# Optimization experiments

Measured on AMD Instinct MI355X. Metric: run time of the kernel, lower is better.

## Reference

```python
import jax, jax.numpy as jnp
import numpy as np

B, S, E, L, H, FF, CB = 16, 1000, 512, 4, 8, 2048, 4096
DH = E // H

def _ln(x, g, b):
    m = x.mean(-1, keepdims=True)
    v = ((x - m) ** 2).mean(-1, keepdims=True)
    return (x - m) / jnp.sqrt(v + 1e-5) * g + b

def setup_inputs() -> dict:
    key = jax.random.key(0)
    cnt = [0]
    def rn(shape, s=0.02):
        cnt[0] += 1
        return jax.random.normal(jax.random.fold_in(key, cnt[0]), shape, jnp.float32) * s
    inp = {}
    inp['noisy_tokens'] = jax.random.randint(jax.random.fold_in(key, 999), (B, S), 0, CB, dtype=jnp.int32)
    inp['codebook'] = rn((CB, E), 1.0)
    # sinusoidal positional encoding, as in _create_positional_encoding
    pe = np.zeros((S, E), np.float32)
    pos = np.arange(S, dtype=np.float32)[:, None]
    div = np.exp(np.arange(0, E, 2, dtype=np.float32) * (-np.log(10000.0) / E))
    pe[:, 0::2] = np.sin(pos * div)
    pe[:, 1::2] = np.cos(pos * div)
    inp['pos_enc'] = jnp.asarray(pe)[None]  # [1,S,E]
    # transformer encoder layers (stacked over L)
    inp['qkv_w'] = rn((L, 3 * E, E)); inp['qkv_b'] = jnp.zeros((L, 3 * E))
    inp['out_w'] = rn((L, E, E));     inp['out_b'] = jnp.zeros((L, E))
    inp['ln1_g'] = jnp.ones((L, E));  inp['ln1_b'] = jnp.zeros((L, E))
    inp['ln2_g'] = jnp.ones((L, E));  inp['ln2_b'] = jnp.zeros((L, E))
    inp['ff1_w'] = rn((L, FF, E));    inp['ff1_b'] = jnp.zeros((L, FF))
    inp['ff2_w'] = rn((L, E, FF));    inp['ff2_b'] = jnp.zeros((L, E))
    inp['fin_g'] = jnp.ones((E,));    inp['fin_b'] = jnp.zeros((E,))
    # post_process: Linear, LN, GELU, Linear
    inp['pp1_w'] = rn((E, E)); inp['pp1_b'] = jnp.zeros((E,))
    inp['pp_ln_g'] = jnp.ones((E,)); inp['pp_ln_b'] = jnp.zeros((E,))
    inp['pp2_w'] = rn((E, E)); inp['pp2_b'] = jnp.zeros((E,))
    inp['res_w'] = jnp.float32(0.1)
    # feature_to_codebook: Linear, LN, GELU, Linear (codebook_dim == E)
    inp['fc1_w'] = rn((E, E)); inp['fc1_b'] = jnp.zeros((E,))
    inp['fc_ln_g'] = jnp.ones((E,)); inp['fc_ln_b'] = jnp.zeros((E,))
    inp['fc2_w'] = rn((E, E)); inp['fc2_b'] = jnp.zeros((E,))
    return inp

def reference(noisy_tokens, codebook, pos_enc, qkv_w, qkv_b, out_w, out_b,
              ln1_g, ln1_b, ln2_g, ln2_b, ff1_w, ff1_b, ff2_w, ff2_b,
              fin_g, fin_b, pp1_w, pp1_b, pp_ln_g, pp_ln_b, pp2_w, pp2_b,
              res_w, fc1_w, fc1_b, fc_ln_g, fc_ln_b, fc2_w, fc2_b):
    gelu = lambda z: jax.nn.gelu(z, approximate=False)
    # token embedding (codebook_projection is Identity) + positional encoding
    x = codebook[noisy_tokens] + pos_enc            # [B,S,E]
    # pre-norm transformer encoder (dropout=0 / eval)
    y = x
    for l in range(L):
        h = _ln(y, ln1_g[l], ln1_b[l])
        qkv = h @ qkv_w[l].T + qkv_b[l]             # [B,S,3E]
        q, k, v = jnp.split(qkv, 3, axis=-1)
        q = q.reshape(B, S, H, DH); k = k.reshape(B, S, H, DH); v = v.reshape(B, S, H, DH)
        scores = jnp.einsum('bqhd,bkhd->bhqk', q, k) / jnp.sqrt(jnp.float32(DH))
        attn = jax.nn.softmax(scores, axis=-1)
        ctx = jnp.einsum('bhqk,bkhd->bqhd', attn, v).reshape(B, S, E)
        y = y + (ctx @ out_w[l].T + out_b[l])
        h2 = _ln(y, ln2_g[l], ln2_b[l])
        y = y + (gelu(h2 @ ff1_w[l].T + ff1_b[l]) @ ff2_w[l].T + ff2_b[l])
    y = _ln(y, fin_g, fin_b)
    # post_process + residual
    pp = gelu(_ln(y @ pp1_w.T + pp1_b, pp_ln_g, pp_ln_b)) @ pp2_w.T + pp2_b
    enhanced = x + res_w * pp
    # feature_to_codebook
    fc = gelu(_ln(enhanced @ fc1_w.T + fc1_b, fc_ln_g, fc_ln_b)) @ fc2_w.T + fc2_b  # [B,S,E]
    # quantize: nearest neighbour in codebook (cdist + argmin)
    flat = fc.reshape(-1, E)
    d2 = (jnp.sum(flat ** 2, -1, keepdims=True)
          - 2.0 * flat @ codebook.T
          + jnp.sum(codebook ** 2, -1))            # [B*S, CB]
    tokens = jnp.argmin(d2, axis=-1).reshape(B, S)
    return fc, tokens
```

## Files before the change

### kernel.cpp

```cpp
#include <hip/hip_runtime.h>
#include <hip/hip_bf16.h>
#include <math.h>

#define NTOK 16000
#define E    512
#define FFD  2048
#define CBN  4096
#define SEQ  1000
#define NH   8
#define VLD  1008

typedef __hip_bfloat16 bf16;
typedef __attribute__((ext_vector_type(8))) short short8;
typedef __attribute__((ext_vector_type(4))) float f32x4;

__device__ __forceinline__ float gelu_f(float v) {
    return 0.5f * v * (1.0f + erff(v * 0.70710678118654752f));
}

__device__ __forceinline__ void split_store(float v, bf16* hi, bf16* lo, size_t idx) {
    bf16 h = __float2bfloat16(v);
    hi[idx] = h;
    lo[idx] = __float2bfloat16(v - __bfloat162float(h));
}

__device__ __forceinline__ void t2_ins(float v, int c, float& v1, int& c1, float& v2, int& c2) {
    const bool b1 = (v < v1) || (v == v1 && c < c1);
    const bool b2 = (v < v2) || (v == v2 && c < c2);
    if (b1) { v2 = v1; c2 = c1; v1 = v; c1 = c; }
    else if (b2) { v2 = v; c2 = c; }
}

__global__ __launch_bounds__(128) void embed_kernel(const int* __restrict__ tok,
                                                    const float* __restrict__ cb,
                                                    const float* __restrict__ pe,
                                                    float* __restrict__ y) {
    const int row = blockIdx.x;
    const int s = row % SEQ;
    const int t = tok[row];
    const int c = threadIdx.x * 4;
    const float4 cv = *(const float4*)(cb + (size_t)t * E + c);
    const float4 pv = *(const float4*)(pe + (size_t)s * E + c);
    *(float4*)(y + (size_t)row * E + c) =
        make_float4(cv.x + pv.x, cv.y + pv.y, cv.z + pv.z, cv.w + pv.w);
}

__global__ __launch_bounds__(256) void split_w(const float* __restrict__ src, int ld,
                                               int cols_log2, int n,
                                               bf16* __restrict__ hi, bf16* __restrict__ lo) {
    const int i = blockIdx.x * 256 + threadIdx.x;
    if (i >= n) return;
    const int r = i >> cols_log2;
    const int c = i & ((1 << cols_log2) - 1);
    const float v = src[(size_t)r * ld + c];
    split_store(v, hi, lo, i);
}

template<int GELU>
__global__ __launch_bounds__(256) void ln_planes(const float* __restrict__ in,
                                                 bf16* __restrict__ hi, bf16* __restrict__ lo,
                                                 const float* __restrict__ g,
                                                 const float* __restrict__ b) {
    const int lane = threadIdx.x & 63;
    const int row = blockIdx.x * 4 + (threadIdx.x >> 6);
    const float* p = in + (size_t)row * E;
    const float4 v0 = *(const float4*)(p + lane * 4);
    const float4 v1 = *(const float4*)(p + 256 + lane * 4);
    float sum = v0.x + v0.y + v0.z + v0.w + v1.x + v1.y + v1.z + v1.w;
    float sq = v0.x * v0.x + v0.y * v0.y + v0.z * v0.z + v0.w * v0.w
             + v1.x * v1.x + v1.y * v1.y + v1.z * v1.z + v1.w * v1.w;
#pragma unroll
    for (int m = 1; m < 64; m <<= 1) {
        sum += __shfl_xor(sum, m);
        sq += __shfl_xor(sq, m);
    }
    const float mean = sum * (1.0f / 512.0f);
    const float var = sq * (1.0f / 512.0f) - mean * mean;
    const float rstd = rsqrtf(var + 1e-5f);
    const float4 g0 = *(const float4*)(g + lane * 4);
    const float4 g1 = *(const float4*)(g + 256 + lane * 4);
    const float4 b0 = *(const float4*)(b + lane * 4);
    const float4 b1 = *(const float4*)(b + 256 + lane * 4);
    const size_t base = (size_t)row * E;
    float o;
    const float vv0[4] = {v0.x, v0.y, v0.z, v0.w};
    const float gg0[4] = {g0.x, g0.y, g0.z, g0.w};
    const float bb0[4] = {b0.x, b0.y, b0.z, b0.w};
    const float vv1[4] = {v1.x, v1.y, v1.z, v1.w};
    const float gg1[4] = {g1.x, g1.y, g1.z, g1.w};
    const float bb1[4] = {b1.x, b1.y, b1.z, b1.w};
#pragma unroll
    for (int t = 0; t < 4; ++t) {
        o = (vv0[t] - mean) * rstd * gg0[t] + bb0[t];
        if (GELU) o = gelu_f(o);
        split_store(o, hi, lo, base + lane * 4 + t);
        o = (vv1[t] - mean) * rstd * gg1[t] + bb1[t];
        if (GELU) o = gelu_f(o);
        split_store(o, hi, lo, base + 256 + lane * 4 + t);
    }
}

template<int OUT>
__global__ __launch_bounds__(256) void gemm_split(
    const bf16* __restrict__ Ah, const bf16* __restrict__ Al, int lda,
    const bf16* __restrict__ Wh, const bf16* __restrict__ Wl, int ldw,
    const float* __restrict__ bias,
    float* __restrict__ C, int ldc,
    bf16* __restrict__ Ohi, bf16* __restrict__ Olo, int ldp,
    const int* __restrict__ noisy, const float* __restrict__ cb,
    const float* __restrict__ pe, const float* __restrict__ resw,
    int K) {
    __shared__ short Ash[2][128][40];
    __shared__ short Wsh[2][128][40];
    const int tid = threadIdx.x;
    const int rowBase = blockIdx.y * 128;
    const int colBase = blockIdx.x * 128;
    const int wave = tid >> 6, lane = tid & 63;
    const int wm = (wave & 1) * 64, wn = (wave >> 1) * 64;
    const int lm = lane & 15;
    const int q8 = (lane >> 4) * 8;
    const int r0 = tid >> 2;
    const int kq = (tid & 3) * 8;

    f32x4 acc[4][4];
#pragma unroll
    for (int i = 0; i < 4; ++i)
#pragma unroll
        for (int j = 0; j < 4; ++j)
            acc[i][j] = (f32x4){0.f, 0.f, 0.f, 0.f};

    for (int k0 = 0; k0 < K; k0 += 32) {
        __syncthreads();
        {
            const size_t a0 = (size_t)(rowBase + r0) * lda + k0 + kq;
            const size_t a1 = (size_t)(rowBase + r0 + 64) * lda + k0 + kq;
            const size_t w0 = (size_t)(colBase + r0) * ldw + k0 + kq;
            const size_t w1 = (size_t)(colBase + r0 + 64) * ldw + k0 + kq;
            *(short8*)&Ash[0][r0][kq]      = *(const short8*)(Ah + a0);
            *(short8*)&Ash[0][r0 + 64][kq] = *(const short8*)(Ah + a1);
            *(short8*)&Ash[1][r0][kq]      = *(const short8*)(Al + a0);
            *(short8*)&Ash[1][r0 + 64][kq] = *(const short8*)(Al + a1);
            *(short8*)&Wsh[0][r0][kq]      = *(const short8*)(Wh + w0);
            *(short8*)&Wsh[0][r0 + 64][kq] = *(const short8*)(Wh + w1);
            *(short8*)&Wsh[1][r0][kq]      = *(const short8*)(Wl + w0);
            *(short8*)&Wsh[1][r0 + 64][kq] = *(const short8*)(Wl + w1);
        }
        __syncthreads();
        short8 ah[4], al[4], wh[4], wl[4];
#pragma unroll
        for (int i = 0; i < 4; ++i) {
            ah[i] = *(const short8*)&Ash[0][wm + i * 16 + lm][q8];
            al[i] = *(const short8*)&Ash[1][wm + i * 16 + lm][q8];
            wh[i] = *(const short8*)&Wsh[0][wn + i * 16 + lm][q8];
            wl[i] = *(const short8*)&Wsh[1][wn + i * 16 + lm][q8];
        }
#pragma unroll
        for (int i = 0; i < 4; ++i)
#pragma unroll
            for (int j = 0; j < 4; ++j)
                acc[i][j] = __builtin_amdgcn_mfma_f32_16x16x32_bf16(ah[i], wh[j], acc[i][j], 0, 0, 0);
#pragma unroll
        for (int i = 0; i < 4; ++i)
#pragma unroll
            for (int j = 0; j < 4; ++j)
                acc[i][j] = __builtin_amdgcn_mfma_f32_16x16x32_bf16(ah[i], wl[j], acc[i][j], 0, 0, 0);
#pragma unroll
        for (int i = 0; i < 4; ++i)
#pragma unroll
            for (int j = 0; j < 4; ++j)
                acc[i][j] = __builtin_amdgcn_mfma_f32_16x16x32_bf16(al[i], wh[j], acc[i][j], 0, 0, 0);
    }

    float bv[4];
#pragma unroll
    for (int j = 0; j < 4; ++j)
        bv[j] = bias ? bias[colBase + wn + j * 16 + lm] : 0.f;
    float scv = 0.f;
    if (OUT == 3) scv = resw[0];
#pragma unroll
    for (int i = 0; i < 4; ++i) {
#pragma unroll
        for (int reg = 0; reg < 4; ++reg) {
            const int r = rowBase + wm + i * 16 + (lane >> 4) * 4 + reg;
            int tok = 0, srow = 0;
            if (OUT == 3) { tok = noisy[r]; srow = r % SEQ; }
#pragma unroll
            for (int j = 0; j < 4; ++j) {
                const int col = colBase + wn + j * 16 + lm;
                float v = acc[i][j][reg] + bv[j];
                if (OUT == 0) {
                    C[(size_t)r * ldc + col] = v;
                } else if (OUT == 1) {
                    float* cp = C + (size_t)r * ldc + col;
                    *cp = *cp + v;
                } else if (OUT == 2) {
                    v = gelu_f(v);
                    split_store(v, Ohi, Olo, (size_t)r * ldp + col);
                } else if (OUT == 3) {
                    const float xv = cb[(size_t)tok * E + col] + pe[(size_t)srow * E + col];
                    v = xv + scv * v;
                    split_store(v, Ohi, Olo, (size_t)r * ldp + col);
                } else {
                    split_store(v, Ohi, Olo, (size_t)r * ldp + col);
                }
            }
        }
    }
}

__global__ __launch_bounds__(256) void vtrans(const bf16* __restrict__ vh_src,
                                              const bf16* __restrict__ vl_src,
                                              bf16* __restrict__ vth,
                                              bf16* __restrict__ vtl) {
    __shared__ short T[64][72];
    const int tid = threadIdx.x;
    const int st = blockIdx.x;
    const int bh = blockIdx.y;
    const int b = bh >> 3, h = bh & 7;
    const int sr = tid >> 2, dq = (tid & 3) * 16;
    const int s_g = st * 64 + sr;
    const int od = tid >> 3;
    const int osq = (tid & 7) * 8;
#pragma unroll
    for (int p = 0; p < 2; ++p) {
        const short* src = (const short*)(p ? vl_src : vh_src);
        short* dst = (short*)(p ? vtl : vth);
        short8 a0 = {0, 0, 0, 0, 0, 0, 0, 0};
        short8 a1 = {0, 0, 0, 0, 0, 0, 0, 0};
        if (s_g < SEQ) {
            const short* sp = src + (size_t)(b * SEQ + s_g) * 1536 + 1024 + h * 64 + dq;
            a0 = *(const short8*)sp;
            a1 = *(const short8*)(sp + 8);
        }
        __syncthreads();
#pragma unroll
        for (int j = 0; j < 8; ++j) T[dq + j][sr] = a0[j];
#pragma unroll
        for (int j = 0; j < 8; ++j) T[dq + 8 + j][sr] = a1[j];
        __syncthreads();
        const int scol = st * 64 + osq;
        if (scol + 8 <= VLD) {
            const short8 o0 = *(const short8*)&T[od][osq];
            const short8 o1 = *(const short8*)&T[od + 32][osq];
            *(short8*)(dst + (size_t)(bh * 64 + od) * VLD + scol) = o0;
            *(short8*)(dst + (size_t)(bh * 64 + od + 32) * VLD + scol) = o1;
        }
    }
}

__global__ __launch_bounds__(256) void attn_mfma(const bf16* __restrict__ qkh,
                                                 const bf16* __restrict__ qkl,
                                                 const bf16* __restrict__ vth,
                                                 const bf16* __restrict__ vtl,
                                                 bf16* __restrict__ chi,
                                                 bf16* __restrict__ clo) {
    __shared__ short QPs[2][64][72];
    __shared__ short Ks[2][64][72];
    __shared__ short Vs[2][64][72];
    const int tid = threadIdx.x;
    const int qt = blockIdx.x, bh = blockIdx.y;
    const int b = bh >> 3, h = bh & 7;
    const int wave = tid >> 6, lane = tid & 63;
    const int lm = lane & 15, g = lane >> 4, q8 = g * 8;
    const int wq = wave * 16;
    const int r0 = tid >> 2, kq = (tid & 3) * 16;

    {
        const int q = qt * 64 + r0;
        short8 z = {0, 0, 0, 0, 0, 0, 0, 0};
        short8 a0 = z, a1 = z, b0 = z, b1 = z;
        if (q < SEQ) {
            const size_t base = (size_t)(b * SEQ + q) * 1536 + h * 64 + kq;
            a0 = *(const short8*)((const short*)qkh + base);
            a1 = *(const short8*)((const short*)qkh + base + 8);
            b0 = *(const short8*)((const short*)qkl + base);
            b1 = *(const short8*)((const short*)qkl + base + 8);
        }
        *(short8*)&QPs[0][r0][kq] = a0; *(short8*)&QPs[0][r0][kq + 8] = a1;
        *(short8*)&QPs[1][r0][kq] = b0; *(short8*)&QPs[1][r0][kq + 8] = b1;
    }
    __syncthreads();
    short8 qfh[2], qfl[2];
#pragma unroll
    for (int t = 0; t < 2; ++t) {
        qfh[t] = *(const short8*)&QPs[0][wq + lm][t * 32 + q8];
        qfl[t] = *(const short8*)&QPs[1][wq + lm][t * 32 + q8];
    }

    float m_i[4] = {-3e38f, -3e38f, -3e38f, -3e38f};
    float l_i[4] = {0.f, 0.f, 0.f, 0.f};
    f32x4 o[4];
#pragma unroll
    for (int dt = 0; dt < 4; ++dt) o[dt] = (f32x4){0.f, 0.f, 0.f, 0.f};

    for (int kb = 0; kb < SEQ; kb += 64) {
        __syncthreads();
        {
            const int kr = kb + r0;
            short8 z = {0, 0, 0, 0, 0, 0, 0, 0};
            short8 a0 = z, a1 = z, b0 = z, b1 = z;
            if (kr < SEQ) {
                const size_t base = (size_t)(b * SEQ + kr) * 1536 + 512 + h * 64 + kq;
                a0 = *(const short8*)((const short*)qkh + base);
                a1 = *(const short8*)((const short*)qkh + base + 8);
                b0 = *(const short8*)((const short*)qkl + base);
                b1 = *(const short8*)((const short*)qkl + base + 8);
            }
            *(short8*)&Ks[0][r0][kq] = a0; *(short8*)&Ks[0][r0][kq + 8] = a1;
            *(short8*)&Ks[1][r0][kq] = b0; *(short8*)&Ks[1][r0][kq + 8] = b1;
            const size_t vbase = (size_t)(bh * 64 + r0) * VLD + kb + kq;
            short8 v0 = z, v1 = z, w0 = z, w1 = z;
            if (kb + kq + 8 <= VLD) {
                v0 = *(const short8*)((const short*)vth + vbase);
                w0 = *(const short8*)((const short*)vtl + vbase);
            }
            if (kb + kq + 16 <= VLD) {
                v1 = *(const short8*)((const short*)vth + vbase + 8);
                w1 = *(const short8*)((const short*)vtl + vbase + 8);
            }
            *(short8*)&Vs[0][r0][kq] = v0; *(short8*)&Vs[0][r0][kq + 8] = v1;
            *(short8*)&Vs[1][r0][kq] = w0; *(short8*)&Vs[1][r0][kq + 8] = w1;
        }
        __syncthreads();
        f32x4 sac[4];
#pragma unroll
        for (int j = 0; j < 4; ++j) sac[j] = (f32x4){0.f, 0.f, 0.f, 0.f};
#pragma unroll
        for (int t = 0; t < 2; ++t) {
#pragma unroll
            for (int j = 0; j < 4; ++j) {
                const short8 kh = *(const short8*)&Ks[0][j * 16 + lm][t * 32 + q8];
                const short8 kl = *(const short8*)&Ks[1][j * 16 + lm][t * 32 + q8];
                sac[j] = __builtin_amdgcn_mfma_f32_16x16x32_bf16(qfh[t], kh, sac[j], 0, 0, 0);
                sac[j] = __builtin_amdgcn_mfma_f32_16x16x32_bf16(qfh[t], kl, sac[j], 0, 0, 0);
                sac[j] = __builtin_amdgcn_mfma_f32_16x16x32_bf16(qfl[t], kh, sac[j], 0, 0, 0);
            }
        }
        float alpha_v[4];
#pragma unroll
        for (int reg = 0; reg < 4; ++reg) {
            float sv[4];
            float rm = -3e38f;
#pragma unroll
            for (int j = 0; j < 4; ++j) {
                const int kc = kb + j * 16 + lm;
                float s = sac[j][reg] * 0.125f;
                s = (kc < SEQ) ? s : -3e38f;
                sv[j] = s;
                rm = fmaxf(rm, s);
            }
#pragma unroll
            for (int m = 1; m < 16; m <<= 1) rm = fmaxf(rm, __shfl_xor(rm, m));
            const float mn = fmaxf(m_i[reg], rm);
            const float al = expf(m_i[reg] - mn);
            float rs = 0.f;
            const int prow = wq + g * 4 + reg;
#pragma unroll
            for (int j = 0; j < 4; ++j) {
                const float pv = expf(sv[j] - mn);
                rs += pv;
                bf16 phb = __float2bfloat16(pv);
                bf16 plb = __float2bfloat16(pv - __bfloat162float(phb));
                QPs[0][prow][j * 16 + lm] = *reinterpret_cast<short*>(&phb);
                QPs[1][prow][j * 16 + lm] = *reinterpret_cast<short*>(&plb);
            }
#pragma unroll
            for (int m = 1; m < 16; m <<= 1) rs += __shfl_xor(rs, m);
            l_i[reg] = l_i[reg] * al + rs;
            m_i[reg] = mn;
            alpha_v[reg] = al;
        }
        const f32x4 av = {alpha_v[0], alpha_v[1], alpha_v[2], alpha_v[3]};
#pragma unroll
        for (int dt = 0; dt < 4; ++dt) o[dt] *= av;
        __syncthreads();
#pragma unroll
        for (int t = 0; t < 2; ++t) {
            const short8 ph = *(const short8*)&QPs[0][wq + lm][t * 32 + q8];
            const short8 pl = *(const short8*)&QPs[1][wq + lm][t * 32 + q8];
#pragma unroll
            for (int dt = 0; dt < 4; ++dt) {
                const short8 vh = *(const short8*)&Vs[0][dt * 16 + lm][t * 32 + q8];
                const short8 vl = *(const short8*)&Vs[1][dt * 16 + lm][t * 32 + q8];
                o[dt] = __builtin_amdgcn_mfma_f32_16x16x32_bf16(ph, vh, o[dt], 0, 0, 0);
                o[dt] = __builtin_amdgcn_mfma_f32_16x16x32_bf16(ph, vl, o[dt], 0, 0, 0);
                o[dt] = __builtin_amdgcn_mfma_f32_16x16x32_bf16(pl, vh, o[dt], 0, 0, 0);
            }
        }
    }
#pragma unroll
    for (int reg = 0; reg < 4; ++reg) {
        const int q = qt * 64 + wq + g * 4 + reg;
        if (q < SEQ) {
            const float inv = 1.0f / l_i[reg];
#pragma unroll
            for (int dt = 0; dt < 4; ++dt) {
                const size_t idx = (size_t)(b * SEQ + q) * E + h * 64 + dt * 16 + lm;
                split_store(o[dt][reg] * inv, chi, clo, idx);
            }
        }
    }
}

__global__ __launch_bounds__(256) void cbnorm_kernel(const float* __restrict__ cb,
                                                     float* __restrict__ out) {
    const int lane = threadIdx.x & 63;
    const int row = blockIdx.x * 4 + (threadIdx.x >> 6);
    const float* p = cb + (size_t)row * E;
    const float4 v0 = *(const float4*)(p + lane * 4);
    const float4 v1 = *(const float4*)(p + 256 + lane * 4);
    float sq = v0.x * v0.x + v0.y * v0.y + v0.z * v0.z + v0.w * v0.w
             + v1.x * v1.x + v1.y * v1.y + v1.z * v1.z + v1.w * v1.w;
#pragma unroll
    for (int m = 1; m < 64; m <<= 1) sq += __shfl_xor(sq, m);
    if (lane == 0) out[row] = sq;
}

__global__ __launch_bounds__(256) void argmin_mfma(
    const bf16* __restrict__ Ah, const bf16* __restrict__ Al,
    const bf16* __restrict__ Wh, const bf16* __restrict__ Wl,
    const float* __restrict__ cbn, float4* __restrict__ part) {
    __shared__ __align__(16) short sbuf[2][2][128][40];
    float4* mrg = reinterpret_cast<float4*>(&sbuf[0][0][0][0]);
    const int tid = threadIdx.x;
    const int rowBase = blockIdx.y * 128;
    const int wave = tid >> 6, lane = tid & 63;
    const int wm = wave * 32;
    const int lm = lane & 15;
    const int g = lane >> 4;
    const int q8 = g * 8;
    const int r0 = tid >> 2;
    const int kq = (tid & 3) * 8;
    const int own_row = tid >> 1;
    const int own_half = tid & 1;

    float rv1 = 3e38f, rv2 = 3e38f;
    int rc1 = 0x7fffffff, rc2 = 0x7fffffff;

    for (int ct = 0; ct < 4; ++ct) {
        const int colBase = blockIdx.x * 512 + ct * 128;
        f32x4 acc[2][8];
#pragma unroll
        for (int i = 0; i < 2; ++i)
#pragma unroll
            for (int j = 0; j < 8; ++j)
                acc[i][j] = (f32x4){0.f, 0.f, 0.f, 0.f};

        for (int k0 = 0; k0 < E; k0 += 32) {
            __syncthreads();
            {
                const size_t a0 = (size_t)(rowBase + r0) * E + k0 + kq;
                const size_t a1 = (size_t)(rowBase + r0 + 64) * E + k0 + kq;
                const size_t w0 = (size_t)(colBase + r0) * E + k0 + kq;
                const size_t w1 = (size_t)(colBase + r0 + 64) * E + k0 + kq;
                *(short8*)&sbuf[0][0][r0][kq]      = *(const short8*)(Ah + a0);
                *(short8*)&sbuf[0][0][r0 + 64][kq] = *(const short8*)(Ah + a1);
                *(short8*)&sbuf[0][1][r0][kq]      = *(const short8*)(Al + a0);
                *(short8*)&sbuf[0][1][r0 + 64][kq] = *(const short8*)(Al + a1);
                *(short8*)&sbuf[1][0][r0][kq]      = *(const short8*)(Wh + w0);
                *(short8*)&sbuf[1][0][r0 + 64][kq] = *(const short8*)(Wh + w1);
                *(short8*)&sbuf[1][1][r0][kq]      = *(const short8*)(Wl + w0);
                *(short8*)&sbuf[1][1][r0 + 64][kq] = *(const short8*)(Wl + w1);
            }
            __syncthreads();
            short8 ah[2], al2[2], wh[8], wl[8];
#pragma unroll
            for (int i = 0; i < 2; ++i) {
                ah[i]  = *(const short8*)&sbuf[0][0][wm + i * 16 + lm][q8];
                al2[i] = *(const short8*)&sbuf[0][1][wm + i * 16 + lm][q8];
            }
#pragma unroll
            for (int j = 0; j < 8; ++j) {
                wh[j] = *(const short8*)&sbuf[1][0][j * 16 + lm][q8];
                wl[j] = *(const short8*)&sbuf[1][1][j * 16 + lm][q8];
            }
#pragma unroll
            for (int i = 0; i < 2; ++i)
#pragma unroll
                for (int j = 0; j < 8; ++j)
                    acc[i][j] = __builtin_amdgcn_mfma_f32_16x16x32_bf16(ah[i], wh[j], acc[i][j], 0, 0, 0);
#pragma unroll
            for (int i = 0; i < 2; ++i)
#pragma unroll
                for (int j = 0; j < 8; ++j)
                    acc[i][j] = __builtin_amdgcn_mfma_f32_16x16x32_bf16(ah[i], wl[j], acc[i][j], 0, 0, 0);
#pragma unroll
            for (int i = 0; i < 2; ++i)
#pragma unroll
                for (int j = 0; j < 8; ++j)
                    acc[i][j] = __builtin_amdgcn_mfma_f32_16x16x32_bf16(al2[i], wh[j], acc[i][j], 0, 0, 0);
        }

        float nv[8];
#pragma unroll
        for (int j = 0; j < 8; ++j) nv[j] = cbn[colBase + j * 16 + lm];
        __syncthreads();
#pragma unroll
        for (int i = 0; i < 2; ++i) {
#pragma unroll
            for (int reg = 0; reg < 4; ++reg) {
                const int row_local = wm + i * 16 + g * 4 + reg;
                float v1 = 3e38f, v2 = 3e38f;
                int c1 = 0x7fffffff, c2 = 0x7fffffff;
#pragma unroll
                for (int j = 0; j < 8; ++j) {
                    const float d = nv[j] - 2.0f * acc[i][j][reg];
                    t2_ins(d, colBase + j * 16 + lm, v1, c1, v2, c2);
                }
                mrg[row_local * 17 + lm] = make_float4(v1, (float)c1, v2, (float)c2);
            }
        }
        __syncthreads();
        {
            float mv1 = 3e38f, mv2 = 3e38f;
            int mc1 = 0x7fffffff, mc2 = 0x7fffffff;
#pragma unroll
            for (int e = 0; e < 8; ++e) {
                const float4 p = mrg[own_row * 17 + own_half * 8 + e];
                t2_ins(p.x, (int)p.y, mv1, mc1, mv2, mc2);
                t2_ins(p.z, (int)p.w, mv1, mc1, mv2, mc2);
            }
            const float pv1 = __shfl_xor(mv1, 1); const int pc1 = __shfl_xor(mc1, 1);
            const float pv2 = __shfl_xor(mv2, 1); const int pc2 = __shfl_xor(mc2, 1);
            t2_ins(pv1, pc1, mv1, mc1, mv2, mc2);
            t2_ins(pv2, pc2, mv1, mc1, mv2, mc2);
            t2_ins(mv1, mc1, rv1, rc1, rv2, rc2);
            t2_ins(mv2, mc2, rv1, rc1, rv2, rc2);
        }
    }
    if (own_half == 0)
        part[(size_t)(rowBase + own_row) * 8 + blockIdx.x] =
            make_float4(rv1, (float)rc1, rv2, (float)rc2);
}

__global__ __launch_bounds__(256) void argmin_exact(const float4* __restrict__ part,
                                                    const float* __restrict__ fc,
                                                    const float* __restrict__ cb,
                                                    const float* __restrict__ cbn,
                                                    float* __restrict__ tokf) {
    const int wave = threadIdx.x >> 6, lane = threadIdx.x & 63;
    const int r = blockIdx.x * 4 + wave;
    float v1 = 3e38f, v2 = 3e38f;
    int c1 = 0x7fffffff, c2 = 0x7fffffff;
    if (lane < 8) {
        const float4 p = part[(size_t)r * 8 + lane];
        v1 = p.x; c1 = (int)p.y; v2 = p.z; c2 = (int)p.w;
    }
#pragma unroll
    for (int m = 1; m < 8; m <<= 1) {
        const float w1 = __shfl_xor(v1, m); const int d1i = __shfl_xor(c1, m);
        const float w2 = __shfl_xor(v2, m); const int d2i = __shfl_xor(c2, m);
        t2_ins(w1, d1i, v1, c1, v2, c2);
        t2_ins(w2, d2i, v1, c1, v2, c2);
    }
    c1 = __shfl(c1, 0);
    c2 = __shfl(c2, 0);
    const float* fr = fc + (size_t)r * E + lane * 8;
    const float* p1 = cb + (size_t)c1 * E + lane * 8;
    const float* p2 = cb + (size_t)c2 * E + lane * 8;
    float d1 = 0.f, d2 = 0.f;
#pragma unroll
    for (int j = 0; j < 8; ++j) {
        const float f = fr[j];
        d1 += f * p1[j];
        d2 += f * p2[j];
    }
#pragma unroll
    for (int m = 1; m < 64; m <<= 1) {
        d1 += __shfl_xor(d1, m);
        d2 += __shfl_xor(d2, m);
    }
    d1 = cbn[c1] - 2.0f * d1;
    d2 = cbn[c2] - 2.0f * d2;
    const int win = ((d1 < d2) || (d1 == d2 && c1 < c2)) ? c1 : c2;
    if (lane == 0) tokf[r] = (float)win;
}

extern "C" void kernel_launch(void* const* d_in, const int* in_sizes, int n_in,
                              void* d_out, int out_size, void* d_ws, size_t ws_size,
                              hipStream_t stream) {
    const int* noisy = (const int*)d_in[0];
    const float* codebook = (const float*)d_in[1];
    const float* pos_enc = (const float*)d_in[2];
    const float* qkv_w = (const float*)d_in[3];
    const float* qkv_b = (const float*)d_in[4];
    const float* out_w = (const float*)d_in[5];
    const float* out_b = (const float*)d_in[6];
    const float* ln1_g = (const float*)d_in[7];
    const float* ln1_b = (const float*)d_in[8];
    const float* ln2_g = (const float*)d_in[9];
    const float* ln2_b = (const float*)d_in[10];
    const float* ff1_w = (const float*)d_in[11];
    const float* ff1_b = (const float*)d_in[12];
    const float* ff2_w = (const float*)d_in[13];
    const float* ff2_b = (const float*)d_in[14];
    const float* fin_g = (const float*)d_in[15];
    const float* fin_b = (const float*)d_in[16];
    const float* pp1_w = (const float*)d_in[17];
    const float* pp1_b = (const float*)d_in[18];
    const float* pp_ln_g = (const float*)d_in[19];
    const float* pp_ln_b = (const float*)d_in[20];
    const float* pp2_w = (const float*)d_in[21];
    const float* pp2_b = (const float*)d_in[22];
    const float* res_w = (const float*)d_in[23];
    const float* fc1_w = (const float*)d_in[24];
    const float* fc1_b = (const float*)d_in[25];
    const float* fc_ln_g = (const float*)d_in[26];
    const float* fc_ln_b = (const float*)d_in[27];
    const float* fc2_w = (const float*)d_in[28];
    const float* fc2_b = (const float*)d_in[29];

    float* ws = (float*)d_ws;
    float* y = ws;
    float* REG = ws + 8192000;
    bf16* qkvh = (bf16*)REG;
    bf16* qkvl = qkvh + 24576000;
    bf16* mid_hi = (bf16*)REG;
    bf16* mid_lo = mid_hi + 16384000;
    float* slotA = REG;
    float* slotB = REG + 8192000;
    bf16* e_hi = (bf16*)slotA;
    bf16* e_lo = e_hi + 8192000;
    float* WV = ws + 32768000;
    bf16* vth = (bf16*)WV;
    bf16* vtl = vth + 8192 * VLD;
    bf16* wA_hi = (bf16*)WV;
    bf16* wA_lo = wA_hi + 1048576;
    bf16* wB_hi = wA_lo + 1048576;
    bf16* wB_lo = wB_hi + 1048576;
    bf16* cbh = wB_lo + 1048576;
    bf16* cbl = cbh + 2097152;
    float* cbn = slotB;
    float4* part = (float4*)(slotB + 4096);
    bf16* h_hi = (bf16*)d_out;
    bf16* h_lo = h_hi + 8192000;
    bf16* fcp_hi = (bf16*)d_out;
    bf16* fcp_lo = fcp_hi + 8192000;
    float* tokf = (float*)d_out + 8192000;

    const dim3 blk(256);
    const dim3 g512(4, 125), g1024(8, 125), g1536(12, 125);

    embed_kernel<<<dim3(NTOK), dim3(128), 0, stream>>>(noisy, codebook, pos_enc, y);

    for (int l = 0; l < 4; ++l) {
        ln_planes<0><<<dim3(4000), blk, 0, stream>>>(y, h_hi, h_lo, ln1_g + l * E, ln1_b + l * E);
        split_w<<<dim3(3072), blk, 0, stream>>>(qkv_w + (size_t)l * 1536 * E, E, 9, 1536 * E, wA_hi, wA_lo);
        gemm_split<4><<<g1536, blk, 0, stream>>>(
            h_hi, h_lo, E, wA_hi, wA_lo, E, qkv_b + (size_t)l * 1536,
            nullptr, 0, qkvh, qkvl, 1536, nullptr, nullptr, nullptr, nullptr, E);
        vtrans<<<dim3(16, 128), blk, 0, stream>>>(qkvh, qkvl, vth, vtl);
        attn_mfma<<<dim3(16, 128), blk, 0, stream>>>(qkvh, qkvl, vth, vtl, h_hi, h_lo);
        split_w<<<dim3(1024), blk, 0, stream>>>(out_w + (size_t)l * E * E, E, 9, E * E, wB_hi, wB_lo);
        gemm_split<1><<<g512, blk, 0, stream>>>(
            h_hi, h_lo, E, wB_hi, wB_lo, E, out_b + (size_t)l * E,
            y, E, nullptr, nullptr, 0, nullptr, nullptr, nullptr, nullptr, E);
        ln_planes<0><<<dim3(4000), blk, 0, stream>>>(y, h_hi, h_lo, ln2_g + l * E, ln2_b + l * E);
        split_w<<<dim3(4096), blk, 0, stream>>>(ff1_w + (size_t)l * FFD * E, E, 9, FFD * E, wA_hi, wA_lo);
        split_w<<<dim3(4096), blk, 0, stream>>>(ff2_w + (size_t)l * E * FFD, FFD, 11, E * FFD, wB_hi, wB_lo);
        for (int c = 0; c < 2; ++c) {
            gemm_split<2><<<g1024, blk, 0, stream>>>(
                h_hi, h_lo, E, wA_hi + (size_t)c * 1024 * E, wA_lo + (size_t)c * 1024 * E, E,
                ff1_b + (size_t)l * FFD + c * 1024,
                nullptr, 0, mid_hi, mid_lo, 1024, nullptr, nullptr, nullptr, nullptr, E);
            gemm_split<1><<<g512, blk, 0, stream>>>(
                mid_hi, mid_lo, 1024, wB_hi + c * 1024, wB_lo + c * 1024, FFD,
                (c == 0) ? (ff2_b + (size_t)l * E) : nullptr,
                y, E, nullptr, nullptr, 0, nullptr, nullptr, nullptr, nullptr, 1024);
        }
    }

    ln_planes<0><<<dim3(4000), blk, 0, stream>>>(y, h_hi, h_lo, fin_g, fin_b);
    split_w<<<dim3(1024), blk, 0, stream>>>(pp1_w, E, 9, E * E, wA_hi, wA_lo);
    gemm_split<0><<<g512, blk, 0, stream>>>(
        h_hi, h_lo, E, wA_hi, wA_lo, E, pp1_b,
        slotB, E, nullptr, nullptr, 0, nullptr, nullptr, nullptr, nullptr, E);
    ln_planes<1><<<dim3(4000), blk, 0, stream>>>(slotB, h_hi, h_lo, pp_ln_g, pp_ln_b);
    split_w<<<dim3(1024), blk, 0, stream>>>(pp2_w, E, 9, E * E, wB_hi, wB_lo);
    gemm_split<3><<<g512, blk, 0, stream>>>(
        h_hi, h_lo, E, wB_hi, wB_lo, E, pp2_b,
        nullptr, 0, e_hi, e_lo, E, noisy, codebook, pos_enc, res_w, E);
    split_w<<<dim3(1024), blk, 0, stream>>>(fc1_w, E, 9, E * E, wA_hi, wA_lo);
    gemm_split<0><<<g512, blk, 0, stream>>>(
        e_hi, e_lo, E, wA_hi, wA_lo, E, fc1_b,
        slotB, E, nullptr, nullptr, 0, nullptr, nullptr, nullptr, nullptr, E);
    ln_planes<1><<<dim3(4000), blk, 0, stream>>>(slotB, h_hi, h_lo, fc_ln_g, fc_ln_b);
    split_w<<<dim3(1024), blk, 0, stream>>>(fc2_w, E, 9, E * E, wB_hi, wB_lo);
    gemm_split<0><<<g512, blk, 0, stream>>>(
        h_hi, h_lo, E, wB_hi, wB_lo, E, fc2_b,
        slotA, E, nullptr, nullptr, 0, nullptr, nullptr, nullptr, nullptr, E);

    split_w<<<dim3(32000), blk, 0, stream>>>(slotA, E, 9, NTOK * E, fcp_hi, fcp_lo);
    split_w<<<dim3(8192), blk, 0, stream>>>(codebook, E, 9, CBN * E, cbh, cbl);
    cbnorm_kernel<<<dim3(1024), blk, 0, stream>>>(codebook, cbn);
    argmin_mfma<<<dim3(8, 125), blk, 0, stream>>>(fcp_hi, fcp_lo, cbh, cbl, cbn, part);
    argmin_exact<<<dim3(4000), blk, 0, stream>>>(part, slotA, codebook, cbn, tokf);
    hipMemcpyAsync(d_out, slotA, (size_t)8192000 * 4, hipMemcpyDeviceToDevice, stream);
}
```

Measured before the change: 3.870 ms.

## Load GEMM tiles via global_load_lds with XOR swizzle; fuse fc2 output split

```diff
diff --git a/kernel.cpp b/kernel.cpp
--- a/kernel.cpp
+++ b/kernel.cpp
@@ -22,6 +22,11 @@
     bf16 h = __float2bfloat16(v);
     hi[idx] = h;
     lo[idx] = __float2bfloat16(v - __bfloat162float(h));
+}
+
+__device__ __forceinline__ void gll16(const bf16* g, short* l) {
+    __builtin_amdgcn_global_load_lds((const __attribute__((address_space(1))) void*)g,
+                                     (__attribute__((address_space(3))) void*)l, 16, 0, 0);
 }
 
 __device__ __forceinline__ void t2_ins(float v, int c, float& v1, int& c1, float& v2, int& c2) {
@@ -110,17 +115,21 @@
     const int* __restrict__ noisy, const float* __restrict__ cb,
     const float* __restrict__ pe, const float* __restrict__ resw,
     int K) {
-    __shared__ short Ash[2][128][40];
-    __shared__ short Wsh[2][128][40];
+    __shared__ __align__(16) short planes[4][128][32];
     const int tid = threadIdx.x;
     const int rowBase = blockIdx.y * 128;
     const int colBase = blockIdx.x * 128;
     const int wave = tid >> 6, lane = tid & 63;
     const int wm = (wave & 1) * 64, wn = (wave >> 1) * 64;
     const int lm = lane & 15;
-    const int q8 = (lane >> 4) * 8;
-    const int r0 = tid >> 2;
-    const int kq = (tid & 3) * 8;
+    const int psl8 = ((lane >> 4) ^ ((lm >> 1) & 3)) * 8;
+
+    const bf16* src = (wave == 0) ? Ah : (wave == 1) ? Al : (wave == 2) ? Wh : Wl;
+    const int sld = (wave < 2) ? lda : ldw;
+    const int srb = (wave < 2) ? rowBase : colBase;
+    const int sslot = (lane & 3) ^ ((lane >> 3) & 3);
+    const bf16* sp = src + (size_t)(srb + (lane >> 2)) * sld + sslot * 8;
+    short* lb = &planes[wave][0][0];
 
     f32x4 acc[4][4];
 #pragma unroll
@@ -132,27 +141,19 @@
     for (int k0 = 0; k0 < K; k0 += 32) {
         __syncthreads();
         {
-            const size_t a0 = (size_t)(rowBase + r0) * lda + k0 + kq;
-            const size_t a1 = (size_t)(rowBase + r0 + 64) * lda + k0 + kq;
-            const size_t w0 = (size_t)(colBase + r0) * ldw + k0 + kq;
-            const size_t w1 = (size_t)(colBase + r0 + 64) * ldw + k0 + kq;
-            *(short8*)&Ash[0][r0][kq]      = *(const short8*)(Ah + a0);
-            *(short8*)&Ash[0][r0 + 64][kq] = *(const short8*)(Ah + a1);
-            *(short8*)&Ash[1][r0][kq]      = *(const short8*)(Al + a0);
-            *(short8*)&Ash[1][r0 + 64][kq] = *(const short8*)(Al + a1);
-            *(short8*)&Wsh[0][r0][kq]      = *(const short8*)(Wh + w0);
-            *(short8*)&Wsh[0][r0 + 64][kq] = *(const short8*)(Wh + w1);
-            *(short8*)&Wsh[1][r0][kq]      = *(const short8*)(Wl + w0);
-            *(short8*)&Wsh[1][r0 + 64][kq] = *(const short8*)(Wl + w1);
+            const bf16* p = sp + k0;
+#pragma unroll
+            for (int j = 0; j < 8; ++j)
+                gll16(p + (size_t)j * 16 * sld, lb + j * 512);
         }
         __syncthreads();
         short8 ah[4], al[4], wh[4], wl[4];
 #pragma unroll
         for (int i = 0; i < 4; ++i) {
-            ah[i] = *(const short8*)&Ash[0][wm + i * 16 + lm][q8];
-            al[i] = *(const short8*)&Ash[1][wm + i * 16 + lm][q8];
-            wh[i] = *(const short8*)&Wsh[0][wn + i * 16 + lm][q8];
-            wl[i] = *(const short8*)&Wsh[1][wn + i * 16 + lm][q8];
+            ah[i] = *(const short8*)&planes[0][wm + i * 16 + lm][psl8];
+            al[i] = *(const short8*)&planes[1][wm + i * 16 + lm][psl8];
+            wh[i] = *(const short8*)&planes[2][wn + i * 16 + lm][psl8];
+            wl[i] = *(const short8*)&planes[3][wn + i * 16 + lm][psl8];
         }
 #pragma unroll
         for (int i = 0; i < 4; ++i)
@@ -200,7 +201,10 @@
                     const float xv = cb[(size_t)tok * E + col] + pe[(size_t)srow * E + col];
                     v = xv + scv * v;
                     split_store(v, Ohi, Olo, (size_t)r * ldp + col);
+                } else if (OUT == 4) {
+                    split_store(v, Ohi, Olo, (size_t)r * ldp + col);
                 } else {
+                    C[(size_t)r * ldc + col] = v;
                     split_store(v, Ohi, Olo, (size_t)r * ldp + col);
                 }
             }
@@ -420,25 +424,29 @@
     const bf16* __restrict__ Ah, const bf16* __restrict__ Al,
     const bf16* __restrict__ Wh, const bf16* __restrict__ Wl,
     const float* __restrict__ cbn, float4* __restrict__ part) {
-    __shared__ __align__(16) short sbuf[2][2][128][40];
-    float4* mrg = reinterpret_cast<float4*>(&sbuf[0][0][0][0]);
+    __shared__ __align__(16) short smem[17408];
+    float4* mrg = reinterpret_cast<float4*>(smem);
     const int tid = threadIdx.x;
     const int rowBase = blockIdx.y * 128;
     const int wave = tid >> 6, lane = tid & 63;
     const int wm = wave * 32;
     const int lm = lane & 15;
     const int g = lane >> 4;
-    const int q8 = g * 8;
-    const int r0 = tid >> 2;
-    const int kq = (tid & 3) * 8;
+    const int psl8 = (g ^ ((lm >> 1) & 3)) * 8;
     const int own_row = tid >> 1;
     const int own_half = tid & 1;
 
+    const bf16* ssrc = (wave == 0) ? Ah : (wave == 1) ? Al : (wave == 2) ? Wh : Wl;
+    const int sslot = (lane & 3) ^ ((lane >> 3) & 3);
+    short* lb = smem + wave * 4096;
+
     float rv1 = 3e38f, rv2 = 3e38f;
     int rc1 = 0x7fffffff, rc2 = 0x7fffffff;
 
     for (int ct = 0; ct < 4; ++ct) {
         const int colBase = blockIdx.x * 512 + ct * 128;
+        const int rb = (wave < 2) ? rowBase : colBase;
+        const bf16* sp = ssrc + (size_t)(rb + (lane >> 2)) * E + sslot * 8;
         f32x4 acc[2][8];
 #pragma unroll
         for (int i = 0; i < 2; ++i)
@@ -449,30 +457,22 @@
         for (int k0 = 0; k0 < E; k0 += 32) {
             __syncthreads();
             {
-                const size_t a0 = (size_t)(rowBase + r0) * E + k0 + kq;
-                const size_t a1 = (size_t)(rowBase + r0 + 64) * E + k0 + kq;
-                const size_t w0 = (size_t)(colBase + r0) * E + k0 + kq;
-                const size_t w1 = (size_t)(colBase + r0 + 64) * E + k0 + kq;
-                *(short8*)&sbuf[0][0][r0][kq]      = *(const short8*)(Ah + a0);
-                *(short8*)&sbuf[0][0][r0 + 64][kq] = *(const short8*)(Ah + a1);
-                *(short8*)&sbuf[0][1][r0][kq]      = *(const short8*)(Al + a0);
-                *(short8*)&sbuf[0][1][r0 + 64][kq] = *(const short8*)(Al + a1);
-                *(short8*)&sbuf[1][0][r0][kq]      = *(const short8*)(Wh + w0);
-                *(short8*)&sbuf[1][0][r0 + 64][kq] = *(const short8*)(Wh + w1);
-                *(short8*)&sbuf[1][1][r0][kq]      = *(const short8*)(Wl + w0);
-                *(short8*)&sbuf[1][1][r0 + 64][kq] = *(const short8*)(Wl + w1);
+                const bf16* p = sp + k0;
+#pragma unroll
+                for (int j = 0; j < 8; ++j)
+                    gll16(p + (size_t)j * 16 * E, lb + j * 512);
             }
             __syncthreads();
             short8 ah[2], al2[2], wh[8], wl[8];
 #pragma unroll
             for (int i = 0; i < 2; ++i) {
-                ah[i]  = *(const short8*)&sbuf[0][0][wm + i * 16 + lm][q8];
-                al2[i] = *(const short8*)&sbuf[0][1][wm + i * 16 + lm][q8];
+                ah[i]  = *(const short8*)(smem + 0 * 4096 + (wm + i * 16 + lm) * 32 + psl8);
+                al2[i] = *(const short8*)(smem + 1 * 4096 + (wm + i * 16 + lm) * 32 + psl8);
             }
 #pragma unroll
             for (int j = 0; j < 8; ++j) {
-                wh[j] = *(const short8*)&sbuf[1][0][j * 16 + lm][q8];
-                wl[j] = *(const short8*)&sbuf[1][1][j * 16 + lm][q8];
+                wh[j] = *(const short8*)(smem + 2 * 4096 + (j * 16 + lm) * 32 + psl8);
+                wl[j] = *(const short8*)(smem + 3 * 4096 + (j * 16 + lm) * 32 + psl8);
             }
 #pragma unroll
             for (int i = 0; i < 2; ++i)
@@ -621,6 +621,8 @@
     float* slotB = REG + 8192000;
     bf16* e_hi = (bf16*)slotA;
     bf16* e_lo = e_hi + 8192000;
+    bf16* fcp2_hi = (bf16*)(REG + 16384000);
+    bf16* fcp2_lo = fcp2_hi + 8192000;
     float* WV = ws + 32768000;
     bf16* vth = (bf16*)WV;
     bf16* vtl = vth + 8192 * VLD;
@@ -634,8 +636,6 @@
     float4* part = (float4*)(slotB + 4096);
     bf16* h_hi = (bf16*)d_out;
     bf16* h_lo = h_hi + 8192000;
-    bf16* fcp_hi = (bf16*)d_out;
-    bf16* fcp_lo = fcp_hi + 8192000;
     float* tokf = (float*)d_out + 8192000;
 
     const dim3 blk(256);
@@ -686,14 +686,13 @@
         slotB, E, nullptr, nullptr, 0, nullptr, nullptr, nullptr, nullptr, E);
     ln_planes<1><<<dim3(4000), blk, 0, stream>>>(slotB, h_hi, h_lo, fc_ln_g, fc_ln_b);
     split_w<<<dim3(1024), blk, 0, stream>>>(fc2_w, E, 9, E * E, wB_hi, wB_lo);
-    gemm_split<0><<<g512, blk, 0, stream>>>(
+    gemm_split<5><<<g512, blk, 0, stream>>>(
         h_hi, h_lo, E, wB_hi, wB_lo, E, fc2_b,
-        slotA, E, nullptr, nullptr, 0, nullptr, nullptr, nullptr, nullptr, E);
-
-    split_w<<<dim3(32000), blk, 0, stream>>>(slotA, E, 9, NTOK * E, fcp_hi, fcp_lo);
+        slotA, E, fcp2_hi, fcp2_lo, E, nullptr, nullptr, nullptr, nullptr, E);
+
     split_w<<<dim3(8192), blk, 0, stream>>>(codebook, E, 9, CBN * E, cbh, cbl);
     cbnorm_kernel<<<dim3(1024), blk, 0, stream>>>(codebook, cbn);
-    argmin_mfma<<<dim3(8, 125), blk, 0, stream>>>(fcp_hi, fcp_lo, cbh, cbl, cbn, part);
+    argmin_mfma<<<dim3(8, 125), blk, 0, stream>>>(fcp2_hi, fcp2_lo, cbh, cbl, cbn, part);
     argmin_exact<<<dim3(4000), blk, 0, stream>>>(part, slotA, codebook, cbn, tokf);
     hipMemcpyAsync(d_out, slotA, (size_t)8192000 * 4, hipMemcpyDeviceToDevice, stream);
 }
```

Result: faster. 3.785 ms (-2.2%).
